# Kernel optimization log

Hardware: AMD Instinct MI355X
Metric: run time of the kernel (lower is better)

Reference implementation:

```python
import jax, jax.numpy as jnp
import numpy as np
from jax import lax

EPS = 1e-5

def _conv_bn(x, w, b, g, be, stride, pad, alpha=0.1):
    # x: [N, Cin, L]; w: [Cout, Cin, K]
    y = lax.conv_general_dilated(x, w, (stride,), [(pad, pad)],
                                 dimension_numbers=('NCH', 'OIH', 'NCH'))
    y = y + b[None, :, None]
    y = jnp.where(y > 0, y, alpha * y)  # LeakyReLU(0.1)
    # BatchNorm1d, training-mode batch stats over (N, L)
    mu = jnp.mean(y, axis=(0, 2), keepdims=True)
    var = jnp.var(y, axis=(0, 2), keepdims=True)
    y = (y - mu) * lax.rsqrt(var + EPS)
    return y * g[None, :, None] + be[None, :, None]

def _forward(x, c, emb, w1, b1, g1, be1, w2, b2, g2, be2, w3, b3, g3, be3,
             w4, b4, g4, be4, w5, b5, g5, be5, fcW, fcb, memK, memV):
    B, S = x.shape
    D = 512  # lstm_size * 32
    e = emb[x]                       # [B, S, 256]
    cf = c.reshape(B * S, c.shape[2])
    ce = emb[cf]                     # [B*S, ctx_len, 256]
    h = _conv_bn(ce, w1, b1, g1, be1, 2, 2)
    h = _conv_bn(h, w2, b2, g2, be2, 2, 2)
    h = _conv_bn(h, w3, b3, g3, be3, 2, 2)
    h = _conv_bn(h, w4, b4, g4, be4, 2, 2)
    h = _conv_bn(h, w5, b5, g5, be5, 1, 0)   # [B*S, 512, 1]
    cfeat = h.reshape(B, S, D)
    # DatabaseMemory: content attention over external DB (vectorized over all
    # 32 per-step slices at once; the original Python loop is stateless per-slice)
    scores = jnp.einsum('bsd,md->bsm', cfeat, memK) / jnp.sqrt(jnp.asarray(D, cfeat.dtype))
    attn = jax.nn.softmax(scores, axis=-1)
    m_out = jnp.einsum('bsm,md->bsd', attn, memV)  # [B, S, 512]
    s = jnp.concatenate([e, cfeat, m_out], axis=2)  # [B, S, 1280]
    logits = jax.nn.softmax(s @ fcW + fcb, axis=2)  # [B, S, vocab]
    return logits

def setup_inputs() -> dict:
    key = jax.random.key(0)
    ks = jax.random.split(key, 12)
    B, S, CTX, V, E = 32, 32, 64, 32000, 256
    d = {}
    d['x'] = jax.random.randint(ks[0], (B, S), 0, V)
    d['c'] = jax.random.randint(ks[1], (B, S, CTX), 0, V)
    d['emb'] = jax.random.normal(ks[2], (V, E), jnp.float32) * 0.02
    convs = [(32, CTX, 8), (64, 32, 8), (128, 64, 8), (256, 128, 8), (512, 256, 14)]
    for i, (co, ci, k) in enumerate(convs, 1):
        kk = jax.random.fold_in(ks[3], i)
        scale = (2.0 / (ci * k)) ** 0.5
        d[f'w{i}'] = jax.random.normal(kk, (co, ci, k), jnp.float32) * scale
        d[f'b{i}'] = jnp.zeros((co,), jnp.float32)
        d[f'g{i}'] = jnp.ones((co,), jnp.float32)
        d[f'be{i}'] = jnp.zeros((co,), jnp.float32)
    d['fcW'] = jax.random.normal(ks[4], (1280, V), jnp.float32) * (1.0 / 1280 ** 0.5)
    d['fcb'] = jnp.zeros((V,), jnp.float32)
    d['memK'] = jax.random.normal(ks[5], (4096, 512), jnp.float32) * 0.05
    d['memV'] = jax.random.normal(ks[6], (4096, 512), jnp.float32) * 0.05
    return d

def reference(x, c, emb, w1, b1, g1, be1, w2, b2, g2, be2, w3, b3, g3, be3,
              w4, b4, g4, be4, w5, b5, g5, be5, fcW, fcb, memK, memV):
    return _forward(x, c, emb, w1, b1, g1, be1, w2, b2, g2, be2, w3, b3, g3,
                    be3, w4, b4, g4, be4, w5, b5, g5, be5, fcW, fcb, memK, memV)
```

## Files before the change

### kernel.cpp

```cpp
#include <hip/hip_runtime.h>
#include <hip/hip_bf16.h>
#include <math.h>


#define N_SAMP 1024

typedef __bf16 bf16x8 __attribute__((ext_vector_type(8)));
typedef __bf16 bf16x4 __attribute__((ext_vector_type(4)));
typedef float  f32x4  __attribute__((ext_vector_type(4)));

__device__ __forceinline__ float blockReduceMax256(float v) {
    __shared__ float sm[4];
    #pragma unroll
    for (int off = 32; off > 0; off >>= 1) v = fmaxf(v, __shfl_down(v, off, 64));
    if ((threadIdx.x & 63) == 0) sm[threadIdx.x >> 6] = v;
    __syncthreads();
    v = fmaxf(fmaxf(sm[0], sm[1]), fmaxf(sm[2], sm[3]));
    __syncthreads();
    return v;
}

__device__ __forceinline__ float blockReduceSum256(float v) {
    __shared__ float sm[4];
    #pragma unroll
    for (int off = 32; off > 0; off >>= 1) v += __shfl_down(v, off, 64);
    if ((threadIdx.x & 63) == 0) sm[threadIdx.x >> 6] = v;
    __syncthreads();
    v = sm[0] + sm[1] + sm[2] + sm[3];
    __syncthreads();
    return v;
}

__global__ __launch_bounds__(256)
void gather_tr_kernel(const int* __restrict__ Cidx, const float* __restrict__ Emb,
                      __bf16* __restrict__ Gt) {
    const int n = blockIdx.x;
    __shared__ int idx[64];
    __shared__ float t[64][65];
    if (threadIdx.x < 64) idx[threadIdx.x] = Cidx[n * 64 + threadIdx.x];
    __bf16* g = Gt + (size_t)n * (262 * 64);
    for (int i = threadIdx.x; i < 6 * 64; i += 256) {
        int r = i >> 6;
        int phys = (r < 2) ? r : r + 256;
        g[(size_t)phys * 64 + (i & 63)] = (__bf16)0.f;
    }
    for (int c0 = 0; c0 < 256; c0 += 64) {
        __syncthreads();
        for (int i = threadIdx.x; i < 4096; i += 256) {
            int ci = i >> 6, li = i & 63;
            t[ci][li] = Emb[(size_t)idx[ci] * 256 + c0 + li];
        }
        __syncthreads();
        for (int i = threadIdx.x; i < 4096; i += 256) {
            int li = i >> 6, ci = i & 63;
            g[(size_t)(2 + c0 + li) * 64 + ci] = (__bf16)t[ci][li];
        }
    }
}

__global__ __launch_bounds__(256)
void wt_kernel(const float* __restrict__ W, __bf16* __restrict__ O,
               int CO, int CI, int KW) {
    const int co = blockIdx.x;
    const int K = CI * KW;
    for (int i = threadIdx.x; i < K; i += 256) {
        int k = i / CI, ci = i - k * CI;
        O[(size_t)co * K + i] =
            (co < CO) ? (__bf16)W[((size_t)co * CI + ci) * KW + k] : (__bf16)0.f;
    }
}

template<int CI, int LIN, int LSTR, int LOUT>
__global__ __launch_bounds__(256)
void im2col_kernel(const float* __restrict__ Y, const float* __restrict__ SS,
                   __bf16* __restrict__ A) {
    constexpr int GPR = CI / 8;
    const int TOT = N_SAMP * LOUT * 8 * GPR;
    int g = blockIdx.x * 256 + threadIdx.x;
    if (g >= TOT) return;
    const int ci0 = (g & (GPR - 1)) * 8;
    const int t = g / GPR;
    const int k = t & 7;
    const int m = t >> 3;
    const int l = m % LOUT;
    const int n = m / LOUT;
    const int li = l * 2 - 2 + k;
    bf16x8 o = {};
    if (li >= 0 && li < LIN) {
        const float* src = Y + ((size_t)n * LSTR + li) * CI + ci0;
        float4 a = *(const float4*)src;
        float4 b = *(const float4*)(src + 4);
        float vv[8] = {a.x, a.y, a.z, a.w, b.x, b.y, b.z, b.w};
        #pragma unroll
        for (int e = 0; e < 8; e++)
            o[e] = (__bf16)fmaf(vv[e], SS[ci0 + e], SS[CI + ci0 + e]);
    }
    *(bf16x8*)(A + (size_t)g * 8) = o;
}

template<int C, int LOUT, int LSTR, int NB>
__global__ __launch_bounds__(256)
void bn_stats_nlc_kernel(const float* __restrict__ Y, float2* __restrict__ partial) {
    constexpr int RPT = 256 / C;
    constexpr int M = N_SAMP * LOUT;
    const int col = threadIdx.x & (C - 1);
    const int rofs = threadIdx.x / C;
    float s = 0.f, s2 = 0.f;
    for (int m = blockIdx.x * RPT + rofs; m < M; m += NB * RPT) {
        float v;
        if constexpr (LSTR == LOUT) {
            v = Y[(size_t)m * C + col];
        } else {
            int n = m / LOUT, l = m - n * LOUT;
            v = Y[((size_t)n * LSTR + l) * C + col];
        }
        s += v; s2 = fmaf(v, v, s2);
    }
    __shared__ float sm[256], sm2[256];
    sm[threadIdx.x] = s; sm2[threadIdx.x] = s2;
    __syncthreads();
    #pragma unroll
    for (int off = 128; off >= C; off >>= 1) {
        if (threadIdx.x < off) {
            sm[threadIdx.x] += sm[threadIdx.x + off];
            sm2[threadIdx.x] += sm2[threadIdx.x + off];
        }
        __syncthreads();
    }
    if (threadIdx.x < C)
        partial[(size_t)blockIdx.x * C + threadIdx.x] =
            make_float2(sm[threadIdx.x], sm2[threadIdx.x]);
}

__global__ __launch_bounds__(64)
void bn_finalize_nlc_kernel(const float2* __restrict__ partial,
                            const float* __restrict__ G, const float* __restrict__ Be,
                            float* __restrict__ SS, int C, int NB, float invCnt) {
    const int c = blockIdx.x;
    float s = 0.f, s2 = 0.f;
    for (int i = threadIdx.x; i < NB; i += 64) {
        float2 p = partial[(size_t)i * C + c];
        s += p.x; s2 += p.y;
    }
    #pragma unroll
    for (int off = 32; off > 0; off >>= 1) {
        s  += __shfl_down(s,  off, 64);
        s2 += __shfl_down(s2, off, 64);
    }
    if (threadIdx.x == 0) {
        double mu  = (double)s * invCnt;
        double var = (double)s2 * invCnt - mu * mu;
        float sc = (float)((double)G[c] / sqrt(var + 1e-5));
        SS[c] = sc;
        SS[C + c] = (float)((double)Be[c] - mu * sc);
    }
}

template<int C, int L, int NB>
__global__ __launch_bounds__(256)
void bn_stats_kernel(const float* __restrict__ Y, float2* __restrict__ partial) {
    constexpr int TOTAL = N_SAMP * L;
    constexpr int PER = (TOTAL + NB - 1) / NB;
    const int c = blockIdx.x, nb = blockIdx.y;
    const int start = nb * PER;
    const int end = (start + PER < TOTAL) ? (start + PER) : TOTAL;
    float s = 0.f, s2 = 0.f;
    for (int i = start + (int)threadIdx.x; i < end; i += 256) {
        const int n = i / L, l = i - n * L;
        const float v = Y[((size_t)n * C + c) * L + l];
        s += v;
        s2 = fmaf(v, v, s2);
    }
    #pragma unroll
    for (int off = 32; off > 0; off >>= 1) {
        s  += __shfl_down(s,  off, 64);
        s2 += __shfl_down(s2, off, 64);
    }
    __shared__ float sm1[4], sm2[4];
    if ((threadIdx.x & 63) == 0) { sm1[threadIdx.x >> 6] = s; sm2[threadIdx.x >> 6] = s2; }
    __syncthreads();
    if (threadIdx.x == 0)
        partial[(size_t)c * NB + nb] =
            make_float2(sm1[0] + sm1[1] + sm1[2] + sm1[3],
                        sm2[0] + sm2[1] + sm2[2] + sm2[3]);
}

__global__ __launch_bounds__(64)
void bn_finalize_kernel(const float2* __restrict__ partial, const float* __restrict__ G,
                        const float* __restrict__ Be, float* __restrict__ SS,
                        int C, int NB, float invCnt) {
    const int c = blockIdx.x;
    float s = 0.f, s2 = 0.f;
    for (int i = threadIdx.x; i < NB; i += 64) {
        float2 p = partial[(size_t)c * NB + i];
        s += p.x; s2 += p.y;
    }
    #pragma unroll
    for (int off = 32; off > 0; off >>= 1) {
        s  += __shfl_down(s,  off, 64);
        s2 += __shfl_down(s2, off, 64);
    }
    if (threadIdx.x == 0) {
        double mu  = (double)s * invCnt;
        double var = (double)s2 * invCnt - mu * mu;
        float sc = (float)((double)G[c] / sqrt(var + 1e-5));
        SS[c] = sc;
        SS[C + c] = (float)((double)Be[c] - mu * sc);
    }
}

__device__ __forceinline__ void gld16(const __bf16* g, __bf16* l) {
    __builtin_amdgcn_global_load_lds(
        (const __attribute__((address_space(1))) unsigned int*)g,
        (__attribute__((address_space(3))) unsigned int*)l, 16, 0, 0);
}

__global__ __launch_bounds__(256)
void mfma_gemm_bt(const __bf16* __restrict__ A, const __bf16* __restrict__ B,
                  const float* __restrict__ bias, float* __restrict__ C,
                  int M, int N, int K, int lda, long long ablk,
                  float scale, int leaky, int swz) {
    __shared__ __bf16 As[128 * 32];
    __shared__ __bf16 Bs[128 * 32];
    const int tid = threadIdx.x;
    int bx = blockIdx.x, by = blockIdx.y;
    if (swz) {
        const int gx = gridDim.x;
        const int G = gx * gridDim.y;
        const int bid = by * gx + bx;
        const int fid = (bid & 7) * (G >> 3) + (bid >> 3);
        bx = fid % gx; by = fid / gx;
    }
    const int row0 = bx * 128;
    const int col0 = by * 128;

    const int r  = tid >> 2;
    const int kb = (tid & 3) * 8;
    const __bf16* Ab = A + (size_t)bx * ablk;
    const __bf16* Ag0 = Ab + (size_t)r * lda + kb;
    const __bf16* Ag1 = Ab + (size_t)(r + 64) * lda + kb;
    const __bf16* Bg0 = B + (size_t)(col0 + r) * K + kb;
    const __bf16* Bg1 = B + (size_t)(col0 + r + 64) * K + kb;
    __bf16* Al0 = As + tid * 8;
    __bf16* Al1 = As + 2048 + tid * 8;
    __bf16* Bl0 = Bs + tid * 8;
    __bf16* Bl1 = Bs + 2048 + tid * 8;

    const int lane = tid & 63;
    const int wave = tid >> 6;
    const int wy = wave >> 1, wx = wave & 1;
    const int l15 = lane & 15, quad = lane >> 4;

    f32x4 acc[4][4] = {};

    for (int k0 = 0; k0 < K; k0 += 32) {
        __syncthreads();
        gld16(Ag0 + k0, Al0);
        gld16(Ag1 + k0, Al1);
        gld16(Bg0 + k0, Bl0);
        gld16(Bg1 + k0, Bl1);
        __syncthreads();

        bf16x8 af[4], bfr[4];
        #pragma unroll
        for (int mi = 0; mi < 4; mi++)
            af[mi] = *(const bf16x8*)&As[(wy * 64 + mi * 16 + l15) * 32 + quad * 8];
        #pragma unroll
        for (int ni = 0; ni < 4; ni++)
            bfr[ni] = *(const bf16x8*)&Bs[(wx * 64 + ni * 16 + l15) * 32 + quad * 8];
        #pragma unroll
        for (int mi = 0; mi < 4; mi++)
            #pragma unroll
            for (int ni = 0; ni < 4; ni++)
                acc[mi][ni] = __builtin_amdgcn_mfma_f32_16x16x32_bf16(
                    af[mi], bfr[ni], acc[mi][ni], 0, 0, 0);
    }

    #pragma unroll
    for (int mi = 0; mi < 4; mi++) {
        #pragma unroll
        for (int ni = 0; ni < 4; ni++) {
            const int col = col0 + wx * 64 + ni * 16 + l15;
            if (col < N) {
                const float bv = bias ? bias[col] : 0.f;
                #pragma unroll
                for (int rg = 0; rg < 4; rg++) {
                    const int row = row0 + wy * 64 + mi * 16 + quad * 4 + rg;
                    float t = acc[mi][ni][rg] * scale + bv;
                    if (leaky) t = t > 0.f ? t : 0.1f * t;
                    C[(size_t)row * N + col] = t;
                }
            }
        }
    }
}

__global__ __launch_bounds__(256)
void cast_bf16_kernel(const float* __restrict__ in, __bf16* __restrict__ out, int n8) {
    int i = blockIdx.x * 256 + threadIdx.x;
    if (i >= n8) return;
    float4 a = ((const float4*)in)[2 * i];
    float4 b = ((const float4*)in)[2 * i + 1];
    bf16x8 v;
    v[0] = (__bf16)a.x; v[1] = (__bf16)a.y; v[2] = (__bf16)a.z; v[3] = (__bf16)a.w;
    v[4] = (__bf16)b.x; v[5] = (__bf16)b.y; v[6] = (__bf16)b.z; v[7] = (__bf16)b.w;
    ((bf16x8*)out)[i] = v;
}

template<int C, int L>
__global__ __launch_bounds__(256)
void bn_apply_cast_kernel(const float* __restrict__ in, __bf16* __restrict__ out,
                          const float* __restrict__ SS, int n8) {
    int i = blockIdx.x * 256 + threadIdx.x;
    if (i >= n8) return;
    float4 a = ((const float4*)in)[2 * i];
    float4 b = ((const float4*)in)[2 * i + 1];
    float vv[8] = {a.x, a.y, a.z, a.w, b.x, b.y, b.z, b.w};
    const int j0 = i * 8;
    bf16x8 v;
    #pragma unroll
    for (int e = 0; e < 8; e++) {
        const int ch = ((j0 + e) / L) % C;
        v[e] = (__bf16)fmaf(vv[e], SS[ch], SS[C + ch]);
    }
    ((bf16x8*)out)[i] = v;
}

__global__ __launch_bounds__(256)
void bn_apply_c512_kernel(float* __restrict__ Y, const float* __restrict__ SS, int n4) {
    int i = blockIdx.x * 256 + threadIdx.x;
    if (i >= n4) return;
    float4 v = ((float4*)Y)[i];
    const int c = (i * 4) & 511;
    v.x = fmaf(v.x, SS[c + 0], SS[512 + c + 0]);
    v.y = fmaf(v.y, SS[c + 1], SS[512 + c + 1]);
    v.z = fmaf(v.z, SS[c + 2], SS[512 + c + 2]);
    v.w = fmaf(v.w, SS[c + 3], SS[512 + c + 3]);
    ((float4*)Y)[i] = v;
}

__global__ __launch_bounds__(256)
void transpose_cast_kernel(const float* __restrict__ in, __bf16* __restrict__ out,
                           int R, int C) {
    __shared__ float t[32][33];
    const int c0 = blockIdx.x * 32, r0 = blockIdx.y * 32;
    const int cc = threadIdx.x & 31, rr = threadIdx.x >> 5;
    #pragma unroll
    for (int i = 0; i < 32; i += 8)
        t[rr + i][cc] = in[(size_t)(r0 + rr + i) * C + c0 + cc];
    __syncthreads();
    #pragma unroll
    for (int i = 0; i < 32; i += 8)
        out[(size_t)(c0 + rr + i) * R + r0 + cc] = (__bf16)t[cc][rr + i];
}

__global__ __launch_bounds__(256)
void softmax4k_kernel(float* __restrict__ P) {
    float* p = P + (size_t)blockIdx.x * 4096;
    float v[16];
    float mx = -INFINITY;
    #pragma unroll
    for (int i = 0; i < 16; i++) {
        v[i] = p[threadIdx.x + i * 256];
        mx = fmaxf(mx, v[i]);
    }
    mx = blockReduceMax256(mx);
    float s = 0.f;
    #pragma unroll
    for (int i = 0; i < 16; i++) { v[i] = __expf(v[i] - mx); s += v[i]; }
    s = blockReduceSum256(s);
    const float inv = 1.f / s;
    #pragma unroll
    for (int i = 0; i < 16; i++) p[threadIdx.x + i * 256] = v[i] * inv;
}

__global__ __launch_bounds__(256)
void softmax_fc_kernel(float* __restrict__ P) {
    float* p = P + (size_t)blockIdx.x * 32000;
    float mx = -INFINITY;
    for (int i = threadIdx.x; i < 32000; i += 256) mx = fmaxf(mx, p[i]);
    mx = blockReduceMax256(mx);
    float s = 0.f;
    for (int i = threadIdx.x; i < 32000; i += 256) {
        float e = __expf(p[i] - mx);
        p[i] = e; s += e;
    }
    s = blockReduceSum256(s);
    const float inv = 1.f / s;
    for (int i = threadIdx.x; i < 32000; i += 256) p[i] *= inv;
}

__global__ __launch_bounds__(320)
void assemble_s_kernel(const int* __restrict__ X, const float* __restrict__ Emb,
                       const float* __restrict__ Cf, const float* __restrict__ Mo,
                       __bf16* __restrict__ S) {
    const int m = blockIdx.x;
    const int col = threadIdx.x * 4;
    float4 v;
    if (col < 256)      v = *(const float4*)(Emb + (size_t)X[m] * 256 + col);
    else if (col < 768) v = *(const float4*)(Cf + (size_t)m * 512 + (col - 256));
    else                v = *(const float4*)(Mo + (size_t)m * 512 + (col - 768));
    bf16x4 o;
    o[0] = (__bf16)v.x; o[1] = (__bf16)v.y; o[2] = (__bf16)v.z; o[3] = (__bf16)v.w;
    *(bf16x4*)(S + (size_t)m * 1280 + col) = o;
}

extern "C" void kernel_launch(void* const* d_in, const int* in_sizes, int n_in,
                              void* d_out, int out_size, void* d_ws, size_t ws_size,
                              hipStream_t stream) {
    const int*   x    = (const int*)d_in[0];
    const int*   c    = (const int*)d_in[1];
    const float* emb  = (const float*)d_in[2];
    const float* w1 = (const float*)d_in[3],  *b1 = (const float*)d_in[4];
    const float* g1 = (const float*)d_in[5],  *be1 = (const float*)d_in[6];
    const float* w2 = (const float*)d_in[7],  *b2 = (const float*)d_in[8];
    const float* g2 = (const float*)d_in[9],  *be2 = (const float*)d_in[10];
    const float* w3 = (const float*)d_in[11], *b3 = (const float*)d_in[12];
    const float* g3 = (const float*)d_in[13], *be3 = (const float*)d_in[14];
    const float* w4 = (const float*)d_in[15], *b4 = (const float*)d_in[16];
    const float* g4 = (const float*)d_in[17], *be4 = (const float*)d_in[18];
    const float* w5 = (const float*)d_in[19], *b5 = (const float*)d_in[20];
    const float* g5 = (const float*)d_in[21], *be5 = (const float*)d_in[22];
    const float* fcW = (const float*)d_in[23], *fcb = (const float*)d_in[24];
    const float* memK = (const float*)d_in[25], *memV = (const float*)d_in[26];
    float* out = (float*)d_out;

    char* W = (char*)d_ws;
    __bf16* fcWT_bf  = (__bf16*)(W + 0);
    __bf16* memK_bf  = (__bf16*)(W + 81920000);
    __bf16* memVT_bf = (__bf16*)(W + 86114304);
    __bf16* w5t      = (__bf16*)(W + 90308608);
    __bf16* w4t      = (__bf16*)(W + 93978624);
    __bf16* w3t      = (__bf16*)(W + 94502912);
    __bf16* w2t      = (__bf16*)(W + 94633984);
    __bf16* w1t      = (__bf16*)(W + 94699520);
    float*  SS       = (float*)(W + 94830592);
    float2* part     = (float2*)(W + 94834688);
    char* P = W + 95358976;
    __bf16* Gt      = (__bf16*)P;
    __bf16* A2      = (__bf16*)P;
    __bf16* A3      = (__bf16*)P;
    __bf16* A4      = (__bf16*)P;
    __bf16* A5      = (__bf16*)P;
    float*  scores  = (float*)P;
    __bf16* attn_bf = (__bf16*)(P + 16777216);
    char* Q = W + 129699840;
    float*  Y1       = (float*)Q;
    float*  Y3       = (float*)Q;
    float*  cfeat    = (float*)Q;
    __bf16* cfeat_bf = (__bf16*)(Q + 2097152);
    float*  m_out    = (float*)(Q + 3145728);
    __bf16* s_bf     = (__bf16*)(Q + 5242880);
    char* R = W + 146477056;
    float*  Y2 = (float*)R;
    float*  Y4 = (float*)R;

    transpose_cast_kernel<<<dim3(1000, 40), 256, 0, stream>>>(fcW, fcWT_bf, 1280, 32000);
    transpose_cast_kernel<<<dim3(16, 128), 256, 0, stream>>>(memV, memVT_bf, 4096, 512);
    cast_bf16_kernel<<<1024, 256, 0, stream>>>(memK, memK_bf, 262144);
    wt_kernel<<<128, 256, 0, stream>>>(w1, w1t, 32, 64, 8);
    wt_kernel<<<128, 256, 0, stream>>>(w2, w2t, 64, 32, 8);
    wt_kernel<<<128, 256, 0, stream>>>(w3, w3t, 128, 64, 8);
    wt_kernel<<<256, 256, 0, stream>>>(w4, w4t, 256, 128, 8);
    wt_kernel<<<512, 256, 0, stream>>>(w5, w5t, 512, 256, 14);

    gather_tr_kernel<<<1024, 256, 0, stream>>>(c, emb, Gt);
    mfma_gemm_bt<<<dim3(1024, 1), 256, 0, stream>>>(Gt, w1t, b1, Y1,
        131072, 32, 512, 128, 16768LL, 1.0f, 1, 0);
    bn_stats_nlc_kernel<32, 127, 128, 512><<<512, 256, 0, stream>>>(Y1, part);
    bn_finalize_nlc_kernel<<<32, 64, 0, stream>>>(part, g1, be1, SS, 32, 512,
                                                  1.0f / (1024.f * 127.f));
    im2col_kernel<32, 127, 128, 62><<<7936, 256, 0, stream>>>(Y1, SS, A2);
    mfma_gemm_bt<<<dim3(496, 1), 256, 0, stream>>>(A2, w2t, b2, Y2,
        63488, 64, 256, 256, 32768LL, 1.0f, 1, 0);
    bn_stats_nlc_kernel<64, 62, 62, 256><<<256, 256, 0, stream>>>(Y2, part);
    bn_finalize_nlc_kernel<<<64, 64, 0, stream>>>(part, g2, be2, SS, 64, 256,
                                                  1.0f / (1024.f * 62.f));
    im2col_kernel<64, 62, 62, 30><<<7680, 256, 0, stream>>>(Y2, SS, A3);
    mfma_gemm_bt<<<dim3(240, 1), 256, 0, stream>>>(A3, w3t, b3, Y3,
        30720, 128, 512, 512, 65536LL, 1.0f, 1, 0);
    bn_stats_nlc_kernel<128, 30, 30, 256><<<256, 256, 0, stream>>>(Y3, part);
    bn_finalize_nlc_kernel<<<128, 64, 0, stream>>>(part, g3, be3, SS, 128, 256,
                                                   1.0f / (1024.f * 30.f));
    im2col_kernel<128, 30, 30, 14><<<7168, 256, 0, stream>>>(Y3, SS, A4);
    mfma_gemm_bt<<<dim3(112, 2), 256, 0, stream>>>(A4, w4t, b4, Y4,
        14336, 256, 1024, 1024, 131072LL, 1.0f, 1, 0);
    bn_stats_nlc_kernel<256, 14, 14, 256><<<256, 256, 0, stream>>>(Y4, part);
    bn_finalize_nlc_kernel<<<256, 64, 0, stream>>>(part, g4, be4, SS, 256, 256,
                                                   1.0f / (1024.f * 14.f));
    bn_apply_cast_kernel<256, 1><<<1792, 256, 0, stream>>>(Y4, A5, SS, 458752);
    mfma_gemm_bt<<<dim3(8, 4), 256, 0, stream>>>(A5, w5t, b5, cfeat,
        1024, 512, 3584, 3584, 458752LL, 1.0f, 1, 1);
    bn_stats_kernel<512, 1, 1><<<dim3(512, 1), 256, 0, stream>>>(cfeat, part);
    bn_finalize_kernel<<<512, 64, 0, stream>>>(part, g5, be5, SS, 512, 1,
                                               1.0f / 1024.f);
    bn_apply_c512_kernel<<<512, 256, 0, stream>>>(cfeat, SS, 131072);

    cast_bf16_kernel<<<256, 256, 0, stream>>>(cfeat, cfeat_bf, 65536);
    mfma_gemm_bt<<<dim3(8, 32), 256, 0, stream>>>(cfeat_bf, memK_bf, nullptr, scores,
        1024, 4096, 512, 512, 65536LL, 0.04419417382415922f, 0, 1);
    softmax4k_kernel<<<1024, 256, 0, stream>>>(scores);
    cast_bf16_kernel<<<2048, 256, 0, stream>>>(scores, attn_bf, 524288);
    mfma_gemm_bt<<<dim3(8, 4), 256, 0, stream>>>(attn_bf, memVT_bf, nullptr, m_out,
        1024, 512, 4096, 4096, 524288LL, 1.0f, 0, 1);

    assemble_s_kernel<<<1024, 320, 0, stream>>>(x, emb, cfeat, m_out, s_bf);
    mfma_gemm_bt<<<dim3(8, 250), 256, 0, stream>>>(s_bf, fcWT_bf, fcb, out,
        1024, 32000, 1280, 1280, 163840LL, 1.0f, 0, 1);
    softmax_fc_kernel<<<1024, 256, 0, stream>>>(out);
}
```

Before: 1.080 ms.

## Fold BN into conv weights, implicit im2col GEMM, split-K, LDS swizzle, online softmax

The BatchNorm scale and shift of each layer are folded into the next conv's weights and bias, and padding rows are pre-filled with values that map to zero. This lets the GEMM read bf16 activations directly through a strided row mapping, which removes the im2col and bn_apply passes. Intermediates are stored as bf16. The small-M GEMMs (conv5 and attn·V) gain split-K with a separate reduce kernel, the GEMM's LDS accesses get an XOR swizzle, and the final softmax switches to a single-pass online max/sum. The trade-offs are extra bf16 rounding of intermediates and of the folded weights, plus several more small kernel launches.

```diff
diff --git a/kernel.cpp b/kernel.cpp
--- a/kernel.cpp
+++ b/kernel.cpp
@@ -59,61 +59,56 @@
 }
 
 __global__ __launch_bounds__(256)
-void wt_kernel(const float* __restrict__ W, __bf16* __restrict__ O,
-               int CO, int CI, int KW) {
+void wt_fold_kernel(const float* __restrict__ W, const float* __restrict__ B,
+                    const float* __restrict__ SS, __bf16* __restrict__ Wt,
+                    float* __restrict__ bias, int CO, int CI, int KW) {
     const int co = blockIdx.x;
     const int K = CI * KW;
-    for (int i = threadIdx.x; i < K; i += 256) {
-        int k = i / CI, ci = i - k * CI;
-        O[(size_t)co * K + i] =
-            (co < CO) ? (__bf16)W[((size_t)co * CI + ci) * KW + k] : (__bf16)0.f;
-    }
-}
-
-template<int CI, int LIN, int LSTR, int LOUT>
-__global__ __launch_bounds__(256)
-void im2col_kernel(const float* __restrict__ Y, const float* __restrict__ SS,
-                   __bf16* __restrict__ A) {
-    constexpr int GPR = CI / 8;
-    const int TOT = N_SAMP * LOUT * 8 * GPR;
-    int g = blockIdx.x * 256 + threadIdx.x;
-    if (g >= TOT) return;
-    const int ci0 = (g & (GPR - 1)) * 8;
-    const int t = g / GPR;
-    const int k = t & 7;
-    const int m = t >> 3;
-    const int l = m % LOUT;
-    const int n = m / LOUT;
-    const int li = l * 2 - 2 + k;
-    bf16x8 o = {};
-    if (li >= 0 && li < LIN) {
-        const float* src = Y + ((size_t)n * LSTR + li) * CI + ci0;
-        float4 a = *(const float4*)src;
-        float4 b = *(const float4*)(src + 4);
-        float vv[8] = {a.x, a.y, a.z, a.w, b.x, b.y, b.z, b.w};
-        #pragma unroll
-        for (int e = 0; e < 8; e++)
-            o[e] = (__bf16)fmaf(vv[e], SS[ci0 + e], SS[CI + ci0 + e]);
-    }
-    *(bf16x8*)(A + (size_t)g * 8) = o;
+    float local = 0.f;
+    if (co < CO) {
+        for (int i = threadIdx.x; i < K; i += 256) {
+            int k = i / CI, ci = i - k * CI;
+            float w = W[((size_t)co * CI + ci) * KW + k];
+            float sc = SS ? SS[ci] : 1.f;
+            Wt[(size_t)co * K + i] = (__bf16)(w * sc);
+            if (SS) local = fmaf(SS[CI + ci], w, local);
+        }
+    } else {
+        for (int i = threadIdx.x; i < K; i += 256)
+            Wt[(size_t)co * K + i] = (__bf16)0.f;
+    }
+    __shared__ float sm[4];
+    #pragma unroll
+    for (int off = 32; off > 0; off >>= 1) local += __shfl_down(local, off, 64);
+    if ((threadIdx.x & 63) == 0) sm[threadIdx.x >> 6] = local;
+    __syncthreads();
+    if (threadIdx.x == 0 && co < CO)
+        bias[co] = B[co] + sm[0] + sm[1] + sm[2] + sm[3];
+}
+
+__global__ __launch_bounds__(256)
+void padfill_kernel(__bf16* __restrict__ Y, const float* __restrict__ SS,
+                    int C, int LSTR, int4 rows, int nrows) {
+    const int n = blockIdx.x;
+    const int rr[4] = {rows.x, rows.y, rows.z, rows.w};
+    for (int i = threadIdx.x; i < nrows * C; i += 256) {
+        int j = i / C, c = i - j * C;
+        float p = -SS[C + c] / SS[c];
+        Y[((size_t)n * LSTR + rr[j]) * C + c] = (__bf16)p;
+    }
 }
 
 template<int C, int LOUT, int LSTR, int NB>
 __global__ __launch_bounds__(256)
-void bn_stats_nlc_kernel(const float* __restrict__ Y, float2* __restrict__ partial) {
+void bn_stats_bf_kernel(const __bf16* __restrict__ Y, float2* __restrict__ partial) {
     constexpr int RPT = 256 / C;
     constexpr int M = N_SAMP * LOUT;
     const int col = threadIdx.x & (C - 1);
     const int rofs = threadIdx.x / C;
     float s = 0.f, s2 = 0.f;
     for (int m = blockIdx.x * RPT + rofs; m < M; m += NB * RPT) {
-        float v;
-        if constexpr (LSTR == LOUT) {
-            v = Y[(size_t)m * C + col];
-        } else {
-            int n = m / LOUT, l = m - n * LOUT;
-            v = Y[((size_t)n * LSTR + l) * C + col];
-        }
+        int n = m / LOUT, l = m - n * LOUT;
+        float v = (float)Y[((size_t)n * LSTR + 2 + l) * C + col];
         s += v; s2 = fmaf(v, v, s2);
     }
     __shared__ float sm[256], sm2[256];
@@ -132,10 +127,24 @@
             make_float2(sm[threadIdx.x], sm2[threadIdx.x]);
 }
 
+__global__ __launch_bounds__(256)
+void bn_stats_cf_kernel(const float* __restrict__ Y, float2* __restrict__ partial) {
+    const int n0 = blockIdx.x * 4;
+    for (int c = threadIdx.x; c < 512; c += 256) {
+        float s = 0.f, s2 = 0.f;
+        #pragma unroll
+        for (int r = 0; r < 4; r++) {
+            float v = Y[(size_t)(n0 + r) * 512 + c];
+            s += v; s2 = fmaf(v, v, s2);
+        }
+        partial[(size_t)blockIdx.x * 512 + c] = make_float2(s, s2);
+    }
+}
+
 __global__ __launch_bounds__(64)
-void bn_finalize_nlc_kernel(const float2* __restrict__ partial,
-                            const float* __restrict__ G, const float* __restrict__ Be,
-                            float* __restrict__ SS, int C, int NB, float invCnt) {
+void bn_finalize_kernel(const float2* __restrict__ partial,
+                        const float* __restrict__ G, const float* __restrict__ Be,
+                        float* __restrict__ SS, int C, int NB, float invCnt) {
     const int c = blockIdx.x;
     float s = 0.f, s2 = 0.f;
     for (int i = threadIdx.x; i < NB; i += 64) {
@@ -156,59 +165,6 @@
     }
 }
 
-template<int C, int L, int NB>
-__global__ __launch_bounds__(256)
-void bn_stats_kernel(const float* __restrict__ Y, float2* __restrict__ partial) {
-    constexpr int TOTAL = N_SAMP * L;
-    constexpr int PER = (TOTAL + NB - 1) / NB;
-    const int c = blockIdx.x, nb = blockIdx.y;
-    const int start = nb * PER;
-    const int end = (start + PER < TOTAL) ? (start + PER) : TOTAL;
-    float s = 0.f, s2 = 0.f;
-    for (int i = start + (int)threadIdx.x; i < end; i += 256) {
-        const int n = i / L, l = i - n * L;
-        const float v = Y[((size_t)n * C + c) * L + l];
-        s += v;
-        s2 = fmaf(v, v, s2);
-    }
-    #pragma unroll
-    for (int off = 32; off > 0; off >>= 1) {
-        s  += __shfl_down(s,  off, 64);
-        s2 += __shfl_down(s2, off, 64);
-    }
-    __shared__ float sm1[4], sm2[4];
-    if ((threadIdx.x & 63) == 0) { sm1[threadIdx.x >> 6] = s; sm2[threadIdx.x >> 6] = s2; }
-    __syncthreads();
-    if (threadIdx.x == 0)
-        partial[(size_t)c * NB + nb] =
-            make_float2(sm1[0] + sm1[1] + sm1[2] + sm1[3],
-                        sm2[0] + sm2[1] + sm2[2] + sm2[3]);
-}
-
-__global__ __launch_bounds__(64)
-void bn_finalize_kernel(const float2* __restrict__ partial, const float* __restrict__ G,
-                        const float* __restrict__ Be, float* __restrict__ SS,
-                        int C, int NB, float invCnt) {
-    const int c = blockIdx.x;
-    float s = 0.f, s2 = 0.f;
-    for (int i = threadIdx.x; i < NB; i += 64) {
-        float2 p = partial[(size_t)c * NB + i];
-        s += p.x; s2 += p.y;
-    }
-    #pragma unroll
-    for (int off = 32; off > 0; off >>= 1) {
-        s  += __shfl_down(s,  off, 64);
-        s2 += __shfl_down(s2, off, 64);
-    }
-    if (threadIdx.x == 0) {
-        double mu  = (double)s * invCnt;
-        double var = (double)s2 * invCnt - mu * mu;
-        float sc = (float)((double)G[c] / sqrt(var + 1e-5));
-        SS[c] = sc;
-        SS[C + c] = (float)((double)Be[c] - mu * sc);
-    }
-}
-
 __device__ __forceinline__ void gld16(const __bf16* g, __bf16* l) {
     __builtin_amdgcn_global_load_lds(
         (const __attribute__((address_space(1))) unsigned int*)g,
@@ -217,9 +173,11 @@
 
 __global__ __launch_bounds__(256)
 void mfma_gemm_bt(const __bf16* __restrict__ A, const __bf16* __restrict__ B,
-                  const float* __restrict__ bias, float* __restrict__ C,
-                  int M, int N, int K, int lda, long long ablk,
-                  float scale, int leaky, int swz) {
+                  const float* __restrict__ bias, void* __restrict__ Cv,
+                  int N, int K, int ksplit,
+                  int lda, int lda2, int rpbl, long long ablk,
+                  int ldc2, long long csplit,
+                  float scale, int leaky, int swz, int cdt) {
     __shared__ __bf16 As[128 * 32];
     __shared__ __bf16 Bs[128 * 32];
     const int tid = threadIdx.x;
@@ -231,16 +189,17 @@
         const int fid = (bid & 7) * (G >> 3) + (bid >> 3);
         bx = fid % gx; by = fid / gx;
     }
-    const int row0 = bx * 128;
     const int col0 = by * 128;
+    const int rpbm = (1 << rpbl) - 1;
 
     const int r  = tid >> 2;
-    const int kb = (tid & 3) * 8;
+    const int kb = (((tid & 3) ^ ((tid >> 3) & 3))) * 8;
+    const int r1 = r + 64;
     const __bf16* Ab = A + (size_t)bx * ablk;
-    const __bf16* Ag0 = Ab + (size_t)r * lda + kb;
-    const __bf16* Ag1 = Ab + (size_t)(r + 64) * lda + kb;
-    const __bf16* Bg0 = B + (size_t)(col0 + r) * K + kb;
-    const __bf16* Bg1 = B + (size_t)(col0 + r + 64) * K + kb;
+    const __bf16* Ag0 = Ab + (size_t)(r  >> rpbl) * lda2 + (size_t)(r  & rpbm) * lda + kb;
+    const __bf16* Ag1 = Ab + (size_t)(r1 >> rpbl) * lda2 + (size_t)(r1 & rpbm) * lda + kb;
+    const __bf16* Bg0 = B + (size_t)(col0 + r ) * K + kb;
+    const __bf16* Bg1 = B + (size_t)(col0 + r1) * K + kb;
     __bf16* Al0 = As + tid * 8;
     __bf16* Al1 = As + 2048 + tid * 8;
     __bf16* Bl0 = Bs + tid * 8;
@@ -250,10 +209,13 @@
     const int wave = tid >> 6;
     const int wy = wave >> 1, wx = wave & 1;
     const int l15 = lane & 15, quad = lane >> 4;
+    const int xq = (quad ^ ((l15 >> 1) & 3)) * 8;
 
     f32x4 acc[4][4] = {};
 
-    for (int k0 = 0; k0 < K; k0 += 32) {
+    const int k0s = blockIdx.z * ksplit;
+    const int k0e = k0s + ksplit;
+    for (int k0 = k0s; k0 < k0e; k0 += 32) {
         __syncthreads();
         gld16(Ag0 + k0, Al0);
         gld16(Ag1 + k0, Al1);
@@ -264,10 +226,10 @@
         bf16x8 af[4], bfr[4];
         #pragma unroll
         for (int mi = 0; mi < 4; mi++)
-            af[mi] = *(const bf16x8*)&As[(wy * 64 + mi * 16 + l15) * 32 + quad * 8];
+            af[mi] = *(const bf16x8*)&As[(wy * 64 + mi * 16 + l15) * 32 + xq];
         #pragma unroll
         for (int ni = 0; ni < 4; ni++)
-            bfr[ni] = *(const bf16x8*)&Bs[(wx * 64 + ni * 16 + l15) * 32 + quad * 8];
+            bfr[ni] = *(const bf16x8*)&Bs[(wx * 64 + ni * 16 + l15) * 32 + xq];
         #pragma unroll
         for (int mi = 0; mi < 4; mi++)
             #pragma unroll
@@ -276,6 +238,8 @@
                     af[mi], bfr[ni], acc[mi][ni], 0, 0, 0);
     }
 
+    const long long cb = (long long)blockIdx.z * csplit
+                       + (long long)bx * (long long)((128 >> rpbl) * ldc2);
     #pragma unroll
     for (int mi = 0; mi < 4; mi++) {
         #pragma unroll
@@ -285,14 +249,44 @@
                 const float bv = bias ? bias[col] : 0.f;
                 #pragma unroll
                 for (int rg = 0; rg < 4; rg++) {
-                    const int row = row0 + wy * 64 + mi * 16 + quad * 4 + rg;
+                    const int row = wy * 64 + mi * 16 + quad * 4 + rg;
+                    const long long a = cb + (long long)(row >> rpbl) * ldc2
+                                      + (long long)(row & rpbm) * N + col;
                     float t = acc[mi][ni][rg] * scale + bv;
                     if (leaky) t = t > 0.f ? t : 0.1f * t;
-                    C[(size_t)row * N + col] = t;
+                    if (cdt) ((__bf16*)Cv)[a] = (__bf16)t;
+                    else     ((float*)Cv)[a] = t;
                 }
             }
         }
     }
+}
+
+__global__ __launch_bounds__(256)
+void splitk_reduce_kernel(const float* __restrict__ P, float* __restrict__ out,
+                          const float* __restrict__ bias, int S, int MN, int N,
+                          int leaky) {
+    int i = blockIdx.x * 256 + threadIdx.x;
+    const int tot = MN >> 2;
+    if (i >= tot) return;
+    float ax = 0.f, ay = 0.f, az = 0.f, aw = 0.f;
+    for (int s = 0; s < S; s++) {
+        float4 p = ((const float4*)(P + (size_t)s * MN))[i];
+        ax += p.x; ay += p.y; az += p.z; aw += p.w;
+    }
+    const int c0 = (i * 4) & (N - 1);
+    float4 o;
+    o.x = ax + (bias ? bias[c0 + 0] : 0.f);
+    o.y = ay + (bias ? bias[c0 + 1] : 0.f);
+    o.z = az + (bias ? bias[c0 + 2] : 0.f);
+    o.w = aw + (bias ? bias[c0 + 3] : 0.f);
+    if (leaky) {
+        o.x = o.x > 0.f ? o.x : 0.1f * o.x;
+        o.y = o.y > 0.f ? o.y : 0.1f * o.y;
+        o.z = o.z > 0.f ? o.z : 0.1f * o.z;
+        o.w = o.w > 0.f ? o.w : 0.1f * o.w;
+    }
+    ((float4*)out)[i] = o;
 }
 
 __global__ __launch_bounds__(256)
@@ -307,27 +301,9 @@
     ((bf16x8*)out)[i] = v;
 }
 
-template<int C, int L>
-__global__ __launch_bounds__(256)
-void bn_apply_cast_kernel(const float* __restrict__ in, __bf16* __restrict__ out,
-                          const float* __restrict__ SS, int n8) {
-    int i = blockIdx.x * 256 + threadIdx.x;
-    if (i >= n8) return;
-    float4 a = ((const float4*)in)[2 * i];
-    float4 b = ((const float4*)in)[2 * i + 1];
-    float vv[8] = {a.x, a.y, a.z, a.w, b.x, b.y, b.z, b.w};
-    const int j0 = i * 8;
-    bf16x8 v;
-    #pragma unroll
-    for (int e = 0; e < 8; e++) {
-        const int ch = ((j0 + e) / L) % C;
-        v[e] = (__bf16)fmaf(vv[e], SS[ch], SS[C + ch]);
-    }
-    ((bf16x8*)out)[i] = v;
-}
-
-__global__ __launch_bounds__(256)
-void bn_apply_c512_kernel(float* __restrict__ Y, const float* __restrict__ SS, int n4) {
+__global__ __launch_bounds__(256)
+void bn_apply_both_kernel(float* __restrict__ Y, __bf16* __restrict__ Yb,
+                          const float* __restrict__ SS, int n4) {
     int i = blockIdx.x * 256 + threadIdx.x;
     if (i >= n4) return;
     float4 v = ((float4*)Y)[i];
@@ -337,6 +313,9 @@
     v.z = fmaf(v.z, SS[c + 2], SS[512 + c + 2]);
     v.w = fmaf(v.w, SS[c + 3], SS[512 + c + 3]);
     ((float4*)Y)[i] = v;
+    bf16x4 o;
+    o[0] = (__bf16)v.x; o[1] = (__bf16)v.y; o[2] = (__bf16)v.z; o[3] = (__bf16)v.w;
+    ((bf16x4*)Yb)[i] = o;
 }
 
 __global__ __launch_bounds__(256)
@@ -377,17 +356,18 @@
 __global__ __launch_bounds__(256)
 void softmax_fc_kernel(float* __restrict__ P) {
     float* p = P + (size_t)blockIdx.x * 32000;
-    float mx = -INFINITY;
-    for (int i = threadIdx.x; i < 32000; i += 256) mx = fmaxf(mx, p[i]);
-    mx = blockReduceMax256(mx);
-    float s = 0.f;
+    float m = -INFINITY, s = 0.f;
     for (int i = threadIdx.x; i < 32000; i += 256) {
-        float e = __expf(p[i] - mx);
-        p[i] = e; s += e;
-    }
-    s = blockReduceSum256(s);
-    const float inv = 1.f / s;
-    for (int i = threadIdx.x; i < 32000; i += 256) p[i] *= inv;
+        float v = p[i];
+        if (v > m) { s = s * __expf(m - v) + 1.f; m = v; }
+        else       { s += __expf(v - m); }
+    }
+    const float M = blockReduceMax256(m);
+    s *= __expf(m - M);
+    const float S = blockReduceSum256(s);
+    const float inv = 1.f / S;
+    for (int i = threadIdx.x; i < 32000; i += 256)
+        p[i] = __expf(p[i] - M) * inv;
 }
 
 __global__ __launch_bounds__(320)
@@ -435,77 +415,83 @@
     __bf16* w2t      = (__bf16*)(W + 94633984);
     __bf16* w1t      = (__bf16*)(W + 94699520);
     float*  SS       = (float*)(W + 94830592);
-    float2* part     = (float2*)(W + 94834688);
-    char* P = W + 95358976;
+    float*  BB       = (float*)(W + 94834688);
+    float2* part     = (float2*)(W + 94836736);
+    __bf16* YA = (__bf16*)(W + 95885312);
+    __bf16* YB = (__bf16*)(W + 104814592);
+    char* P = W + 114268160;
     __bf16* Gt      = (__bf16*)P;
-    __bf16* A2      = (__bf16*)P;
-    __bf16* A3      = (__bf16*)P;
-    __bf16* A4      = (__bf16*)P;
-    __bf16* A5      = (__bf16*)P;
+    float*  Pc5     = (float*)P;
     float*  scores  = (float*)P;
     __bf16* attn_bf = (__bf16*)(P + 16777216);
-    char* Q = W + 129699840;
-    float*  Y1       = (float*)Q;
-    float*  Y3       = (float*)Q;
-    float*  cfeat    = (float*)Q;
-    __bf16* cfeat_bf = (__bf16*)(Q + 2097152);
-    float*  m_out    = (float*)(Q + 3145728);
-    __bf16* s_bf     = (__bf16*)(Q + 5242880);
-    char* R = W + 146477056;
-    float*  Y2 = (float*)R;
-    float*  Y4 = (float*)R;
+    float*  Pmo     = (float*)(P + 25165824);
+    float*  cfeat    = (float*)(W + 148609024);
+    __bf16* cfeat_bf = (__bf16*)(W + 150706176);
+    float*  m_out    = (float*)(W + 151754752);
+    __bf16* s_bf     = (__bf16*)(W + 153851904);
+
+    __bf16* Y1 = YA; __bf16* Y3 = YA;
+    __bf16* Y2 = YB; __bf16* Y4 = YB;
 
     transpose_cast_kernel<<<dim3(1000, 40), 256, 0, stream>>>(fcW, fcWT_bf, 1280, 32000);
     transpose_cast_kernel<<<dim3(16, 128), 256, 0, stream>>>(memV, memVT_bf, 4096, 512);
     cast_bf16_kernel<<<1024, 256, 0, stream>>>(memK, memK_bf, 262144);
-    wt_kernel<<<128, 256, 0, stream>>>(w1, w1t, 32, 64, 8);
-    wt_kernel<<<128, 256, 0, stream>>>(w2, w2t, 64, 32, 8);
-    wt_kernel<<<128, 256, 0, stream>>>(w3, w3t, 128, 64, 8);
-    wt_kernel<<<256, 256, 0, stream>>>(w4, w4t, 256, 128, 8);
-    wt_kernel<<<512, 256, 0, stream>>>(w5, w5t, 512, 256, 14);
-
+    wt_fold_kernel<<<128, 256, 0, stream>>>(w1, b1, nullptr, w1t, BB, 32, 64, 8);
     gather_tr_kernel<<<1024, 256, 0, stream>>>(c, emb, Gt);
-    mfma_gemm_bt<<<dim3(1024, 1), 256, 0, stream>>>(Gt, w1t, b1, Y1,
-        131072, 32, 512, 128, 16768LL, 1.0f, 1, 0);
-    bn_stats_nlc_kernel<32, 127, 128, 512><<<512, 256, 0, stream>>>(Y1, part);
-    bn_finalize_nlc_kernel<<<32, 64, 0, stream>>>(part, g1, be1, SS, 32, 512,
-                                                  1.0f / (1024.f * 127.f));
-    im2col_kernel<32, 127, 128, 62><<<7936, 256, 0, stream>>>(Y1, SS, A2);
-    mfma_gemm_bt<<<dim3(496, 1), 256, 0, stream>>>(A2, w2t, b2, Y2,
-        63488, 64, 256, 256, 32768LL, 1.0f, 1, 0);
-    bn_stats_nlc_kernel<64, 62, 62, 256><<<256, 256, 0, stream>>>(Y2, part);
-    bn_finalize_nlc_kernel<<<64, 64, 0, stream>>>(part, g2, be2, SS, 64, 256,
-                                                  1.0f / (1024.f * 62.f));
-    im2col_kernel<64, 62, 62, 30><<<7680, 256, 0, stream>>>(Y2, SS, A3);
-    mfma_gemm_bt<<<dim3(240, 1), 256, 0, stream>>>(A3, w3t, b3, Y3,
-        30720, 128, 512, 512, 65536LL, 1.0f, 1, 0);
-    bn_stats_nlc_kernel<128, 30, 30, 256><<<256, 256, 0, stream>>>(Y3, part);
-    bn_finalize_nlc_kernel<<<128, 64, 0, stream>>>(part, g3, be3, SS, 128, 256,
-                                                   1.0f / (1024.f * 30.f));
-    im2col_kernel<128, 30, 30, 14><<<7168, 256, 0, stream>>>(Y3, SS, A4);
-    mfma_gemm_bt<<<dim3(112, 2), 256, 0, stream>>>(A4, w4t, b4, Y4,
-        14336, 256, 1024, 1024, 131072LL, 1.0f, 1, 0);
-    bn_stats_nlc_kernel<256, 14, 14, 256><<<256, 256, 0, stream>>>(Y4, part);
-    bn_finalize_nlc_kernel<<<256, 64, 0, stream>>>(part, g4, be4, SS, 256, 256,
-                                                   1.0f / (1024.f * 14.f));
-    bn_apply_cast_kernel<256, 1><<<1792, 256, 0, stream>>>(Y4, A5, SS, 458752);
-    mfma_gemm_bt<<<dim3(8, 4), 256, 0, stream>>>(A5, w5t, b5, cfeat,
-        1024, 512, 3584, 3584, 458752LL, 1.0f, 1, 1);
-    bn_stats_kernel<512, 1, 1><<<dim3(512, 1), 256, 0, stream>>>(cfeat, part);
-    bn_finalize_kernel<<<512, 64, 0, stream>>>(part, g5, be5, SS, 512, 1,
+
+    mfma_gemm_bt<<<dim3(1024, 1), 256, 0, stream>>>(Gt, w1t, BB, Y1 + 64,
+        32, 512, 512, 128, 0, 7, 16768LL, 4160, 0LL, 1.0f, 1, 0, 1);
+    bn_stats_bf_kernel<32, 127, 130, 512><<<512, 256, 0, stream>>>(Y1, part);
+    bn_finalize_kernel<<<32, 64, 0, stream>>>(part, g1, be1, SS, 32, 512,
+                                              1.0f / (1024.f * 127.f));
+    padfill_kernel<<<1024, 256, 0, stream>>>(Y1, SS, 32, 130,
+                                             make_int4(0, 1, 129, 0), 3);
+    wt_fold_kernel<<<128, 256, 0, stream>>>(w2, b2, SS, w2t, BB, 64, 32, 8);
+
+    mfma_gemm_bt<<<dim3(512, 1), 256, 0, stream>>>(Y1, w2t, BB, Y2 + 128,
+        64, 256, 256, 64, 4160, 6, 8320LL, 4224, 0LL, 1.0f, 1, 0, 1);
+    bn_stats_bf_kernel<64, 62, 66, 256><<<256, 256, 0, stream>>>(Y2, part);
+    bn_finalize_kernel<<<64, 64, 0, stream>>>(part, g2, be2, SS, 64, 256,
+                                              1.0f / (1024.f * 62.f));
+    padfill_kernel<<<1024, 256, 0, stream>>>(Y2, SS, 64, 66,
+                                             make_int4(0, 1, 64, 65), 4);
+    wt_fold_kernel<<<128, 256, 0, stream>>>(w3, b3, SS, w3t, BB, 128, 64, 8);
+
+    mfma_gemm_bt<<<dim3(256, 1), 256, 0, stream>>>(Y2, w3t, BB, Y3 + 256,
+        128, 512, 512, 128, 4224, 5, 16896LL, 4352, 0LL, 1.0f, 1, 0, 1);
+    bn_stats_bf_kernel<128, 30, 34, 256><<<256, 256, 0, stream>>>(Y3, part);
+    bn_finalize_kernel<<<128, 64, 0, stream>>>(part, g3, be3, SS, 128, 256,
+                                               1.0f / (1024.f * 30.f));
+    padfill_kernel<<<1024, 256, 0, stream>>>(Y3, SS, 128, 34,
+                                             make_int4(0, 1, 32, 33), 4);
+    wt_fold_kernel<<<256, 256, 0, stream>>>(w4, b4, SS, w4t, BB, 256, 128, 8);
+
+    mfma_gemm_bt<<<dim3(128, 2), 256, 0, stream>>>(Y3, w4t, BB, Y4 + 512,
+        256, 1024, 1024, 256, 4352, 4, 34816LL, 4608, 0LL, 1.0f, 1, 0, 1);
+    bn_stats_bf_kernel<256, 14, 18, 256><<<256, 256, 0, stream>>>(Y4, part);
+    bn_finalize_kernel<<<256, 64, 0, stream>>>(part, g4, be4, SS, 256, 256,
+                                               1.0f / (1024.f * 14.f));
+    wt_fold_kernel<<<512, 256, 0, stream>>>(w5, b5, SS, w5t, BB, 512, 256, 14);
+
+    mfma_gemm_bt<<<dim3(8, 4, 8), 256, 0, stream>>>(Y4 + 512, w5t, nullptr, Pc5,
+        512, 3584, 448, 4608, 0, 7, 589824LL, 65536, 524288LL, 1.0f, 0, 0, 0);
+    splitk_reduce_kernel<<<512, 256, 0, stream>>>(Pc5, cfeat, BB, 8, 524288, 512, 1);
+    bn_stats_cf_kernel<<<256, 256, 0, stream>>>(cfeat, part);
+    bn_finalize_kernel<<<512, 64, 0, stream>>>(part, g5, be5, SS, 512, 256,
                                                1.0f / 1024.f);
-    bn_apply_c512_kernel<<<512, 256, 0, stream>>>(cfeat, SS, 131072);
-
-    cast_bf16_kernel<<<256, 256, 0, stream>>>(cfeat, cfeat_bf, 65536);
+    bn_apply_both_kernel<<<512, 256, 0, stream>>>(cfeat, cfeat_bf, SS, 131072);
+
     mfma_gemm_bt<<<dim3(8, 32), 256, 0, stream>>>(cfeat_bf, memK_bf, nullptr, scores,
-        1024, 4096, 512, 512, 65536LL, 0.04419417382415922f, 0, 1);
+        4096, 512, 512, 512, 0, 7, 65536LL, 524288, 0LL,
+        0.04419417382415922f, 0, 1, 0);
     softmax4k_kernel<<<1024, 256, 0, stream>>>(scores);
     cast_bf16_kernel<<<2048, 256, 0, stream>>>(scores, attn_bf, 524288);
-    mfma_gemm_bt<<<dim3(8, 4), 256, 0, stream>>>(attn_bf, memVT_bf, nullptr, m_out,
-        1024, 512, 4096, 4096, 524288LL, 1.0f, 0, 1);
+    mfma_gemm_bt<<<dim3(8, 4, 4), 256, 0, stream>>>(attn_bf, memVT_bf, nullptr, Pmo,
+        512, 4096, 1024, 4096, 0, 7, 524288LL, 65536, 524288LL, 1.0f, 0, 0, 0);
+    splitk_reduce_kernel<<<512, 256, 0, stream>>>(Pmo, m_out, nullptr, 4, 524288, 512, 0);
 
     assemble_s_kernel<<<1024, 320, 0, stream>>>(x, emb, cfeat, m_out, s_bf);
     mfma_gemm_bt<<<dim3(8, 250), 256, 0, stream>>>(s_bf, fcWT_bf, fcb, out,
-        1024, 32000, 1280, 1280, 163840LL, 1.0f, 0, 1);
+        32000, 1280, 1280, 1280, 0, 7, 163840LL, 4096000, 0LL, 1.0f, 0, 1, 0);
     softmax_fc_kernel<<<1024, 256, 0, stream>>>(out);
 }
```

New measurement: 950.3 us. 1.14x faster.
